# Kernel optimization log

Hardware: AMD Instinct MI355X
Metric: run time of the kernel (lower is better)

## Reference

```python
import jax, jax.numpy as jnp
import numpy as np
from jax import lax

T_LEN, BATCH, D_IN, D_HID, N_LAYERS = 512, 32, 512, 512, 4


def setup_inputs() -> dict:
    key = jax.random.key(0)
    kx, kw, ku = jax.random.split(key, 3)
    x = jax.random.normal(kx, (T_LEN, BATCH, D_IN), dtype=jnp.float32)
    # xavier-ish scale on input kernels to keep the relu recurrence stable
    W = jax.random.normal(kw, (N_LAYERS, D_HID, D_IN), dtype=jnp.float32) * (1.0 / np.sqrt(D_IN))
    b = jnp.zeros((N_LAYERS, D_HID), dtype=jnp.float32)
    # diagonal recurrent weights in [0,1) so |u|<=1 (non-exploding)
    u = jax.random.uniform(ku, (N_LAYERS, D_HID), dtype=jnp.float32)
    return {"x": x, "W": W, "b": b, "u": u}


def _indrnn_layer(x, W_l, b_l, u_l):
    # x: [T, B, Din]; precompute input projection as one big GEMM
    xh = jnp.einsum('tbd,hd->tbh', x, W_l) + b_l  # [T, B, Dh]
    h0 = jnp.zeros((x.shape[1], W_l.shape[0]), dtype=x.dtype)

    def step(h, xh_t):
        h_new = jax.nn.relu(xh_t + u_l * h)
        return h_new, h_new

    _, outs = lax.scan(step, h0, xh)
    return outs  # [T, B, Dh]


def reference(x, W, b, u):
    out = x
    for l in range(W.shape[0]):  # fixed small layer count
        out = _indrnn_layer(out, W[l], b[l], u[l])
    return out
```

## Files before the change

kernel.cpp:

```cpp
#include <hip/hip_runtime.h>
#include <hip/hip_bf16.h>

typedef short bf16x8 __attribute__((ext_vector_type(8)));
typedef float f32x4 __attribute__((ext_vector_type(4)));

#define T_LEN 512
#define BATCH 32
#define D 512
#define M_TOT (T_LEN * BATCH)
#define NLAYER 4

#define BM 128
#define BN 128
#define BK 64
#define NT (D / BK)
#define EP 72

#define QBN 64
#define QWROWS 32
#define QBM 256
#define QB_ELEMS (QBN * D)
#define QA_SLOT (QWROWS * BK)
#define QSMEM_BYTES ((QB_ELEMS + 8 * 2 * QA_SLOT) * 2)
#define QEP 72

#define CH 32
#define NCH (T_LEN / CH)

#define SBAR()                             \
    do {                                   \
        __builtin_amdgcn_s_barrier();      \
        __builtin_amdgcn_sched_barrier(0); \
    } while (0)
#define VMCNT(n)                                              \
    do {                                                      \
        asm volatile("s_waitcnt vmcnt(" #n ")" ::: "memory"); \
        __builtin_amdgcn_sched_barrier(0);                    \
    } while (0)
#define LGKM0()                                               \
    do {                                                      \
        asm volatile("s_waitcnt lgkmcnt(0)" ::: "memory");    \
        __builtin_amdgcn_sched_barrier(0);                    \
    } while (0)

__global__ __launch_bounds__(256) void convert_k(const float* __restrict__ W,
                                                 __hip_bfloat16* __restrict__ Wb) {
    const int i = (blockIdx.x * 256 + threadIdx.x) * 4;
    float4 v = *(const float4*)(W + i);
    __hip_bfloat16 h0 = __float2bfloat16(v.x);
    __hip_bfloat16 h1 = __float2bfloat16(v.y);
    __hip_bfloat16 h2 = __float2bfloat16(v.z);
    __hip_bfloat16 h3 = __float2bfloat16(v.w);
    ushort4 o;
    o.x = *(const unsigned short*)&h0;
    o.y = *(const unsigned short*)&h1;
    o.z = *(const unsigned short*)&h2;
    o.w = *(const unsigned short*)&h3;
    *(ushort4*)(Wb + i) = o;
}

__global__ __launch_bounds__(256) void gemm_l0(const float* __restrict__ Agf0,
                                               const __hip_bfloat16* __restrict__ Bt,
                                               const float* __restrict__ bias,
                                               __hip_bfloat16* __restrict__ Cb) {
    constexpr int K = D;
    constexpr int N = D;
    __shared__ __hip_bfloat16 smem[4 * BM * BK];
    __hip_bfloat16* const AsP[2] = {smem, smem + BM * BK};
    __hip_bfloat16* const BsP[2] = {smem + 2 * BM * BK, smem + 3 * BM * BK};

    const int tid  = threadIdx.x;
    const int wave = tid >> 6;
    const int lane = tid & 63;

    const int bid = blockIdx.x;
    const int xcd = bid & 7;
    const int jb  = bid >> 3;
    const int bm  = xcd * 16 + (jb >> 2);
    const int bn  = jb & 3;

    const int wm = (wave >> 1) * 64;
    const int wn = (wave & 1) * 64;

    const int srow = lane >> 3;
    const int scol = ((lane & 7) ^ srow) * 8;

    const float* Agf = Agf0 + (size_t)(bm * BM) * K;
    const __hip_bfloat16* Bg = Bt + (size_t)(bn * BN) * K;

    f32x4 acc[4][4] = {};
    float4 va[4][2];

#define STAGE_B0(buf, k0)                                                                            \
    do {                                                                                             \
        _Pragma("unroll") for (int jj = 0; jj < 4; ++jj) {                                           \
            const int rbase = (jj * 4 + wave) * 8;                                                   \
            __builtin_amdgcn_global_load_lds(                                                        \
                (const __attribute__((address_space(1))) void*)(Bg + (size_t)(rbase + srow) * K + (k0) + scol), \
                (__attribute__((address_space(3))) void*)(&BsP[buf][rbase * BK]), 16, 0, 0);         \
        }                                                                                            \
    } while (0)

#define LOAD_A0(k0)                                                                                  \
    do {                                                                                             \
        _Pragma("unroll") for (int jj = 0; jj < 4; ++jj) {                                           \
            const int rbase = (jj * 4 + wave) * 8;                                                   \
            const float* s = Agf + (size_t)(rbase + srow) * K + (k0) + scol;                         \
            va[jj][0] = *(const float4*)s;                                                           \
            va[jj][1] = *(const float4*)(s + 4);                                                     \
        }                                                                                            \
    } while (0)

#define WRITE_A0(buf)                                                                                \
    do {                                                                                             \
        _Pragma("unroll") for (int jj = 0; jj < 4; ++jj) {                                           \
            const int rbase = (jj * 4 + wave) * 8;                                                   \
            bf16x8 pk;                                                                               \
            _Pragma("unroll") for (int q = 0; q < 4; ++q) {                                          \
                __hip_bfloat16 t0 = __float2bfloat16(((const float*)&va[jj][0])[q]);                 \
                __hip_bfloat16 t1 = __float2bfloat16(((const float*)&va[jj][1])[q]);                 \
                pk[q]     = *(const short*)&t0;                                                      \
                pk[q + 4] = *(const short*)&t1;                                                      \
            }                                                                                        \
            *(bf16x8*)(&AsP[buf][(rbase + srow) * BK + (lane & 7) * 8]) = pk;                        \
        }                                                                                            \
    } while (0)

#define COMPUTE0(buf)                                                                                \
    do {                                                                                             \
        bf16x8 af[4][2], bv[4][2];                                                                   \
        const int fr = lane & 15;                                                                    \
        const int kq = lane >> 4;                                                                    \
        _Pragma("unroll") for (int mi = 0; mi < 4; ++mi) {                                           \
            const int r = wm + mi * 16 + fr;                                                         \
            _Pragma("unroll") for (int kh = 0; kh < 2; ++kh) {                                       \
                const int c = ((kh * 4 + kq) ^ (fr & 7)) * 8;                                        \
                af[mi][kh] = *(const bf16x8*)(&AsP[buf][r * BK + c]);                                \
            }                                                                                        \
        }                                                                                            \
        _Pragma("unroll") for (int ni = 0; ni < 4; ++ni) {                                           \
            const int r = wn + ni * 16 + fr;                                                         \
            _Pragma("unroll") for (int kh = 0; kh < 2; ++kh) {                                       \
                const int c = ((kh * 4 + kq) ^ (fr & 7)) * 8;                                        \
                bv[ni][kh] = *(const bf16x8*)(&BsP[buf][r * BK + c]);                                \
            }                                                                                        \
        }                                                                                            \
        _Pragma("unroll") for (int kh = 0; kh < 2; ++kh)                                             \
            _Pragma("unroll") for (int mi = 0; mi < 4; ++mi)                                         \
                _Pragma("unroll") for (int ni = 0; ni < 4; ++ni)                                     \
                    acc[mi][ni] = __builtin_amdgcn_mfma_f32_16x16x32_bf16(af[mi][kh], bv[ni][kh],    \
                                                                          acc[mi][ni], 0, 0, 0);    \
    } while (0)

    LOAD_A0(0);
    STAGE_B0(0, 0);
    WRITE_A0(0);
    __syncthreads();
    int cur = 0;
#pragma unroll
    for (int kt = 1; kt < NT; ++kt) {
        LOAD_A0(kt * BK);
        STAGE_B0(cur ^ 1, kt * BK);
        COMPUTE0(cur);
        WRITE_A0(cur ^ 1);
        __syncthreads();
        cur ^= 1;
    }
    COMPUTE0(cur);
    __syncthreads();

    {
        __hip_bfloat16* S = smem + wave * (64 * EP);
        const int cfr = lane & 15;
        const int cfq = lane >> 4;
        float bs[4];
#pragma unroll
        for (int ni = 0; ni < 4; ++ni) bs[ni] = bias[bn * BN + wn + ni * 16 + cfr];
#pragma unroll
        for (int mi = 0; mi < 4; ++mi)
#pragma unroll
            for (int ni = 0; ni < 4; ++ni)
#pragma unroll
                for (int r = 0; r < 4; ++r)
                    S[(mi * 16 + cfq * 4 + r) * EP + ni * 16 + cfr] =
                        __float2bfloat16(acc[mi][ni][r] + bs[ni]);
        const int rq = lane >> 3;
        const int cl = (lane & 7) * 8;
#pragma unroll
        for (int p = 0; p < 8; ++p) {
            const int lr = p * 8 + rq;
            bf16x8 v = *(const bf16x8*)(S + lr * EP + cl);
            *(bf16x8*)(&Cb[(size_t)(bm * BM + wm + lr) * N + bn * BN + wn + cl]) = v;
        }
    }
#undef STAGE_B0
#undef LOAD_A0
#undef WRITE_A0
#undef COMPUTE0
}

__global__ __launch_bounds__(512) void gemm_resB(const __hip_bfloat16* __restrict__ A,
                                                 const __hip_bfloat16* __restrict__ Bt,
                                                 const float* __restrict__ bias,
                                                 __hip_bfloat16* __restrict__ Cb) {
    constexpr int K = D;
    constexpr int N = D;
    extern __shared__ __hip_bfloat16 smem[];

    const int tid  = threadIdx.x;
    const int wave = tid >> 6;
    const int lane = tid & 63;

    const int bid = blockIdx.x;
    const int xcd = bid & 7;
    const int jb  = bid >> 3;
    const int bm  = xcd * 8 + (jb >> 3);
    const int bn  = jb & 7;

    __hip_bfloat16* const Bsm = smem;
    __hip_bfloat16* const Awv = smem + QB_ELEMS + wave * (2 * QA_SLOT);

    const int srow = lane >> 3;
    const int sch  = lane & 7;

    const __hip_bfloat16* Agw = A + (size_t)(bm * QBM + wave * QWROWS) * K;
    const __hip_bfloat16* Bg  = Bt + (size_t)(bn * QBN) * K;

    f32x4 acc[2][4] = {};

#pragma unroll
    for (int p = 0; p < 8; ++p) {
        const int row = p * 8 + wave;
        const int sc  = ((lane & ~7) | ((lane & 7) ^ (row & 7))) * 8;
        __builtin_amdgcn_global_load_lds(
            (const __attribute__((address_space(1))) void*)(Bg + (size_t)row * K + sc),
            (__attribute__((address_space(3))) void*)(Bsm + row * D), 16, 0, 0);
    }
#define STAGE_A(slot, k0)                                                                            \
    do {                                                                                             \
        _Pragma("unroll") for (int jj = 0; jj < 4; ++jj) {                                           \
            const int rbase = jj * 8;                                                                \
            __builtin_amdgcn_global_load_lds(                                                        \
                (const __attribute__((address_space(1))) void*)(Agw + (size_t)(rbase + srow) * K + (k0) + (sch ^ srow) * 8), \
                (__attribute__((address_space(3))) void*)(Awv + (slot) * QA_SLOT + rbase * BK), 16, 0, 0); \
        }                                                                                            \
    } while (0)

    STAGE_A(0, 0);
    STAGE_A(1, BK);
    VMCNT(4);
    SBAR();

    const int fr = lane & 15;
    const int kq = lane >> 4;

#pragma unroll
    for (int t = 0; t < NT; ++t) {
        if (t > 0) {
            if (t < NT - 1) {
                VMCNT(4);
            } else {
                VMCNT(0);
            }
        }
        const __hip_bfloat16* Asl = Awv + (t & 1) * QA_SLOT;
        bf16x8 af[2][2], bv[4][2];
#pragma unroll
        for (int mi = 0; mi < 2; ++mi)
#pragma unroll
            for (int kh = 0; kh < 2; ++kh) {
                const int c = ((kh * 4 + kq) ^ (fr & 7)) * 8;
                af[mi][kh] = *(const bf16x8*)(&Asl[(mi * 16 + fr) * BK + c]);
            }
#pragma unroll
        for (int ni = 0; ni < 4; ++ni)
#pragma unroll
            for (int kh = 0; kh < 2; ++kh) {
                const int n = ni * 16 + fr;
                const int c = t * BK + (((kh * 4 + kq) ^ (fr & 7)) * 8);
                bv[ni][kh] = *(const bf16x8*)(&Bsm[n * D + c]);
            }
        LGKM0();
        if (t + 2 < NT) STAGE_A(t & 1, (t + 2) * BK);
        __builtin_amdgcn_sched_barrier(0);
        __builtin_amdgcn_s_setprio(1);
#pragma unroll
        for (int kh = 0; kh < 2; ++kh)
#pragma unroll
            for (int mi = 0; mi < 2; ++mi)
#pragma unroll
                for (int ni = 0; ni < 4; ++ni)
                    acc[mi][ni] = __builtin_amdgcn_mfma_f32_16x16x32_bf16(af[mi][kh], bv[ni][kh],
                                                                          acc[mi][ni], 0, 0, 0);
        __builtin_amdgcn_s_setprio(0);
    }
#undef STAGE_A

    {
        __hip_bfloat16* S = Awv;
        const int cfr = lane & 15;
        const int cfq = lane >> 4;
        float bs[4];
#pragma unroll
        for (int ni = 0; ni < 4; ++ni) bs[ni] = bias[bn * QBN + ni * 16 + cfr];
#pragma unroll
        for (int mi = 0; mi < 2; ++mi)
#pragma unroll
            for (int ni = 0; ni < 4; ++ni)
#pragma unroll
                for (int r = 0; r < 4; ++r)
                    S[(mi * 16 + cfq * 4 + r) * QEP + ni * 16 + cfr] =
                        __float2bfloat16(acc[mi][ni][r] + bs[ni]);
        const int rq = lane >> 3;
        const int cl = (lane & 7) * 8;
#pragma unroll
        for (int p = 0; p < 4; ++p) {
            const int lr = p * 8 + rq;
            bf16x8 v = *(const bf16x8*)(S + lr * QEP + cl);
            *(bf16x8*)(&Cb[(size_t)(bm * QBM + wave * QWROWS + lr) * N + bn * QBN + cl]) = v;
        }
    }
}

template <int MODE>
__global__ __launch_bounds__(512) void scan_k(const __hip_bfloat16* __restrict__ xh,
                                              const float* __restrict__ u,
                                              float* __restrict__ outf,
                                              __hip_bfloat16* __restrict__ outb) {
    __shared__ float4 md[NCH][32];
    const int i2  = threadIdx.x & 31;
    const int c   = threadIdx.x >> 5;
    const int idx = blockIdx.x * 64 + i2 * 2;
    const float u0 = u[idx & (D - 1)];
    const float u1 = u[(idx + 1) & (D - 1)];

    const __hip_bfloat16* p = xh + (size_t)c * CH * M_TOT + idx;
    unsigned int xv[CH];
#pragma unroll
    for (int t = 0; t < CH; ++t) xv[t] = *(const unsigned int*)(p + (size_t)t * M_TOT);

    float m0 = 0.f, d0 = 0.f, m1 = 0.f, d1 = 0.f;
#pragma unroll
    for (int t = 0; t < CH; ++t) {
        const float a0 = __uint_as_float(xv[t] << 16);
        const float a1 = __uint_as_float(xv[t] & 0xffff0000u);
        m0 = fmaxf(fmaf(u0, m0, a0), 0.f);
        d0 = fmaf(u0, d0, a0);
        m1 = fmaxf(fmaf(u1, m1, a1), 0.f);
        d1 = fmaf(u1, d1, a1);
    }
    md[c][i2] = make_float4(m0, d0, m1, d1);
    __syncthreads();

    float e0 = u0 * u0, e1 = u1 * u1;
    e0 *= e0; e0 *= e0; e0 *= e0; e0 *= e0;
    e1 *= e1; e1 *= e1; e1 *= e1; e1 *= e1;
    float h0 = 0.f, h1 = 0.f;
    for (int jj = 0; jj < c; ++jj) {
        const float4 v = md[jj][i2];
        h0 = fmaxf(v.x, fmaf(e0, h0, v.y));
        h1 = fmaxf(v.z, fmaf(e1, h1, v.w));
    }

    const size_t base = (size_t)c * CH * M_TOT + idx;
#pragma unroll
    for (int t = 0; t < CH; ++t) {
        const size_t off = base + (size_t)t * M_TOT;
        const float a0 = __uint_as_float(xv[t] << 16);
        const float a1 = __uint_as_float(xv[t] & 0xffff0000u);
        h0 = fmaxf(fmaf(u0, h0, a0), 0.f);
        h1 = fmaxf(fmaf(u1, h1, a1), 0.f);
        if (MODE & 1) *(float2*)(outf + off) = make_float2(h0, h1);
        if (MODE & 2) {
            __hip_bfloat16 b0 = __float2bfloat16(h0);
            __hip_bfloat16 b1 = __float2bfloat16(h1);
            unsigned int pk = (unsigned int)(*(unsigned short*)&b0) |
                              ((unsigned int)(*(unsigned short*)&b1) << 16);
            *(unsigned int*)(outb + off) = pk;
        }
    }
}

extern "C" void kernel_launch(void* const* d_in, const int* in_sizes, int n_in,
                              void* d_out, int out_size, void* d_ws, size_t ws_size,
                              hipStream_t stream) {
    const float* x = (const float*)d_in[0];
    const float* W = (const float*)d_in[1];
    const float* b = (const float*)d_in[2];
    const float* u = (const float*)d_in[3];
    float* out = (float*)d_out;

    __hip_bfloat16* Wb = (__hip_bfloat16*)d_ws;
    __hip_bfloat16* Ab = (__hip_bfloat16*)((char*)d_ws + (size_t)NLAYER * D * D * 2);
    __hip_bfloat16* Xh = Ab + (size_t)M_TOT * D;

    (void)hipFuncSetAttribute((const void*)gemm_resB,
                              hipFuncAttributeMaxDynamicSharedMemorySize, QSMEM_BYTES);

    convert_k<<<(NLAYER * D * D / 4) / 256, 256, 0, stream>>>(W, Wb);

    for (int l = 0; l < NLAYER; ++l) {
        if (l == 0) {
            gemm_l0<<<(M_TOT / BM) * (D / BN), 256, 0, stream>>>(x, Wb, b, Xh);
        } else {
            gemm_resB<<<(M_TOT / QBM) * (D / QBN), 512, QSMEM_BYTES, stream>>>(
                Ab, Wb + (size_t)l * D * D, b + (size_t)l * D, Xh);
        }
        if (l < NLAYER - 1) {
            scan_k<2><<<M_TOT / 64, 512, 0, stream>>>(Xh, u + (size_t)l * D, nullptr, Ab);
        } else {
            scan_k<1><<<M_TOT / 64, 512, 0, stream>>>(Xh, u + (size_t)l * D, out, nullptr);
        }
    }
}
```

Measured before the change: 113.6 us.

## Load GEMM A operand straight to registers with triple-buffered prefetch

In the gemm_resB kernel used for layers 1–3, the A operand is no longer staged through LDS. It is now loaded directly from global memory into registers, with a three-slot software prefetch. The block M tile doubles to 512 rows, so each wave computes 64 rows and the grid drops to 256 blocks. Shared memory now holds only the B tile, and the output staging reuses it after a barrier. This removes the LDS round trip and waitcnt choreography for A. The cost is higher register pressure, less coalesced per-lane global loads, and fewer blocks to hide latency.

Result: slower. 147.5 us (+29.9%).

```diff
diff --git a/kernel.cpp b/kernel.cpp
--- a/kernel.cpp
+++ b/kernel.cpp
@@ -17,31 +17,11 @@
 #define EP 72
 
 #define QBN 64
-#define QWROWS 32
-#define QBM 256
-#define QB_ELEMS (QBN * D)
-#define QA_SLOT (QWROWS * BK)
-#define QSMEM_BYTES ((QB_ELEMS + 8 * 2 * QA_SLOT) * 2)
+#define QBM 512
 #define QEP 72
 
 #define CH 32
 #define NCH (T_LEN / CH)
-
-#define SBAR()                             \
-    do {                                   \
-        __builtin_amdgcn_s_barrier();      \
-        __builtin_amdgcn_sched_barrier(0); \
-    } while (0)
-#define VMCNT(n)                                              \
-    do {                                                      \
-        asm volatile("s_waitcnt vmcnt(" #n ")" ::: "memory"); \
-        __builtin_amdgcn_sched_barrier(0);                    \
-    } while (0)
-#define LGKM0()                                               \
-    do {                                                      \
-        asm volatile("s_waitcnt lgkmcnt(0)" ::: "memory");    \
-        __builtin_amdgcn_sched_barrier(0);                    \
-    } while (0)
 
 __global__ __launch_bounds__(256) void convert_k(const float* __restrict__ W,
                                                  __hip_bfloat16* __restrict__ Wb) {
@@ -205,7 +185,7 @@
                                                  __hip_bfloat16* __restrict__ Cb) {
     constexpr int K = D;
     constexpr int N = D;
-    extern __shared__ __hip_bfloat16 smem[];
+    __shared__ __hip_bfloat16 Bsm[QBN * D];
 
     const int tid  = threadIdx.x;
     const int wave = tid >> 6;
@@ -214,110 +194,94 @@
     const int bid = blockIdx.x;
     const int xcd = bid & 7;
     const int jb  = bid >> 3;
-    const int bm  = xcd * 8 + (jb >> 3);
+    const int bm  = xcd * 4 + (jb >> 3);
     const int bn  = jb & 7;
 
-    __hip_bfloat16* const Bsm = smem;
-    __hip_bfloat16* const Awv = smem + QB_ELEMS + wave * (2 * QA_SLOT);
-
-    const int srow = lane >> 3;
-    const int sch  = lane & 7;
-
-    const __hip_bfloat16* Agw = A + (size_t)(bm * QBM + wave * QWROWS) * K;
     const __hip_bfloat16* Bg  = Bt + (size_t)(bn * QBN) * K;
-
-    f32x4 acc[2][4] = {};
-
-#pragma unroll
-    for (int p = 0; p < 8; ++p) {
-        const int row = p * 8 + wave;
+    const __hip_bfloat16* Agw = A + (size_t)(bm * QBM + wave * 64) * K;
+
+    const int fr = lane & 15;
+    const int kq = lane >> 4;
+
+#pragma unroll
+    for (int jj = 0; jj < 8; ++jj) {
+        const int row = wave * 8 + jj;
         const int sc  = ((lane & ~7) | ((lane & 7) ^ (row & 7))) * 8;
         __builtin_amdgcn_global_load_lds(
             (const __attribute__((address_space(1))) void*)(Bg + (size_t)row * K + sc),
             (__attribute__((address_space(3))) void*)(Bsm + row * D), 16, 0, 0);
     }
-#define STAGE_A(slot, k0)                                                                            \
-    do {                                                                                             \
-        _Pragma("unroll") for (int jj = 0; jj < 4; ++jj) {                                           \
-            const int rbase = jj * 8;                                                                \
-            __builtin_amdgcn_global_load_lds(                                                        \
-                (const __attribute__((address_space(1))) void*)(Agw + (size_t)(rbase + srow) * K + (k0) + (sch ^ srow) * 8), \
-                (__attribute__((address_space(3))) void*)(Awv + (slot) * QA_SLOT + rbase * BK), 16, 0, 0); \
-        }                                                                                            \
-    } while (0)
-
-    STAGE_A(0, 0);
-    STAGE_A(1, BK);
-    VMCNT(4);
-    SBAR();
-
-    const int fr = lane & 15;
-    const int kq = lane >> 4;
+
+    bf16x8 ap[3][4][2];
+    f32x4 acc[4][4] = {};
+
+#define LOADA(slot, t)                                                                               \
+    do {                                                                                             \
+        _Pragma("unroll") for (int mi = 0; mi < 4; ++mi)                                             \
+            _Pragma("unroll") for (int kh = 0; kh < 2; ++kh)                                         \
+                ap[slot][mi][kh] = *(const bf16x8*)(Agw + (size_t)(mi * 16 + fr) * K +               \
+                                                    (t) * BK + kh * 32 + kq * 8);                    \
+    } while (0)
+
+    LOADA(0, 0);
+    LOADA(1, 1);
+    __syncthreads();
 
 #pragma unroll
     for (int t = 0; t < NT; ++t) {
-        if (t > 0) {
-            if (t < NT - 1) {
-                VMCNT(4);
-            } else {
-                VMCNT(0);
+        __builtin_amdgcn_sched_barrier(0);
+        if (t + 2 < NT) LOADA((t + 2) % 3, t + 2);
+        bf16x8 bv[4][2];
+#pragma unroll
+        for (int ni = 0; ni < 4; ++ni)
+#pragma unroll
+            for (int kh = 0; kh < 2; ++kh) {
+                const int r = ni * 16 + fr;
+                const int c = t * BK + (((kh * 4 + kq) ^ (fr & 7)) * 8);
+                bv[ni][kh] = *(const bf16x8*)(&Bsm[r * D + c]);
             }
-        }
-        const __hip_bfloat16* Asl = Awv + (t & 1) * QA_SLOT;
-        bf16x8 af[2][2], bv[4][2];
-#pragma unroll
-        for (int mi = 0; mi < 2; ++mi)
-#pragma unroll
-            for (int kh = 0; kh < 2; ++kh) {
-                const int c = ((kh * 4 + kq) ^ (fr & 7)) * 8;
-                af[mi][kh] = *(const bf16x8*)(&Asl[(mi * 16 + fr) * BK + c]);
-            }
-#pragma unroll
-        for (int ni = 0; ni < 4; ++ni)
-#pragma unroll
-            for (int kh = 0; kh < 2; ++kh) {
-                const int n = ni * 16 + fr;
-                const int c = t * BK + (((kh * 4 + kq) ^ (fr & 7)) * 8);
-                bv[ni][kh] = *(const bf16x8*)(&Bsm[n * D + c]);
-            }
-        LGKM0();
-        if (t + 2 < NT) STAGE_A(t & 1, (t + 2) * BK);
-        __builtin_amdgcn_sched_barrier(0);
         __builtin_amdgcn_s_setprio(1);
 #pragma unroll
         for (int kh = 0; kh < 2; ++kh)
 #pragma unroll
-            for (int mi = 0; mi < 2; ++mi)
+            for (int mi = 0; mi < 4; ++mi)
 #pragma unroll
                 for (int ni = 0; ni < 4; ++ni)
-                    acc[mi][ni] = __builtin_amdgcn_mfma_f32_16x16x32_bf16(af[mi][kh], bv[ni][kh],
-                                                                          acc[mi][ni], 0, 0, 0);
+                    acc[mi][ni] = __builtin_amdgcn_mfma_f32_16x16x32_bf16(
+                        ap[t % 3][mi][kh], bv[ni][kh], acc[mi][ni], 0, 0, 0);
         __builtin_amdgcn_s_setprio(0);
     }
-#undef STAGE_A
+#undef LOADA
+
+    __syncthreads();
 
     {
-        __hip_bfloat16* S = Awv;
-        const int cfr = lane & 15;
+        __hip_bfloat16* S = Bsm + wave * (32 * QEP);
         const int cfq = lane >> 4;
         float bs[4];
 #pragma unroll
-        for (int ni = 0; ni < 4; ++ni) bs[ni] = bias[bn * QBN + ni * 16 + cfr];
-#pragma unroll
-        for (int mi = 0; mi < 2; ++mi)
-#pragma unroll
-            for (int ni = 0; ni < 4; ++ni)
-#pragma unroll
-                for (int r = 0; r < 4; ++r)
-                    S[(mi * 16 + cfq * 4 + r) * QEP + ni * 16 + cfr] =
-                        __float2bfloat16(acc[mi][ni][r] + bs[ni]);
-        const int rq = lane >> 3;
-        const int cl = (lane & 7) * 8;
-#pragma unroll
-        for (int p = 0; p < 4; ++p) {
-            const int lr = p * 8 + rq;
-            bf16x8 v = *(const bf16x8*)(S + lr * QEP + cl);
-            *(bf16x8*)(&Cb[(size_t)(bm * QBM + wave * QWROWS + lr) * N + bn * QBN + cl]) = v;
+        for (int ni = 0; ni < 4; ++ni) bs[ni] = bias[bn * QBN + ni * 16 + fr];
+#pragma unroll
+        for (int h = 0; h < 2; ++h) {
+#pragma unroll
+            for (int mi2 = 0; mi2 < 2; ++mi2) {
+                const int mi = h * 2 + mi2;
+#pragma unroll
+                for (int ni = 0; ni < 4; ++ni)
+#pragma unroll
+                    for (int r = 0; r < 4; ++r)
+                        S[(mi2 * 16 + cfq * 4 + r) * QEP + ni * 16 + fr] =
+                            __float2bfloat16(acc[mi][ni][r] + bs[ni]);
+            }
+            const int rq = lane >> 3;
+            const int cl = (lane & 7) * 8;
+#pragma unroll
+            for (int p = 0; p < 4; ++p) {
+                const int lr = p * 8 + rq;
+                bf16x8 v = *(const bf16x8*)(S + lr * QEP + cl);
+                *(bf16x8*)(&Cb[(size_t)(bm * QBM + wave * 64 + h * 32 + lr) * N +
+                               bn * QBN + cl]) = v;
+            }
         }
     }
 }
@@ -394,16 +358,13 @@
     __hip_bfloat16* Ab = (__hip_bfloat16*)((char*)d_ws + (size_t)NLAYER * D * D * 2);
     __hip_bfloat16* Xh = Ab + (size_t)M_TOT * D;
 
-    (void)hipFuncSetAttribute((const void*)gemm_resB,
-                              hipFuncAttributeMaxDynamicSharedMemorySize, QSMEM_BYTES);
-
     convert_k<<<(NLAYER * D * D / 4) / 256, 256, 0, stream>>>(W, Wb);
 
     for (int l = 0; l < NLAYER; ++l) {
         if (l == 0) {
             gemm_l0<<<(M_TOT / BM) * (D / BN), 256, 0, stream>>>(x, Wb, b, Xh);
         } else {
-            gemm_resB<<<(M_TOT / QBM) * (D / QBN), 512, QSMEM_BYTES, stream>>>(
+            gemm_resB<<<(M_TOT / QBM) * (D / QBN), 512, 0, stream>>>(
                 Ab, Wb + (size_t)l * D * D, b + (size_t)l * D, Xh);
         }
         if (l < NLAYER - 1) {
```
